# Optimization experiments

Measured on AMD Instinct MI355X. Metric: run time of the kernel, lower is better.

Reference implementation:

```python
import jax, jax.numpy as jnp
import numpy as np

B, N, D, H = 256, 100000, 512, 2048

def setup_inputs() -> dict:
    key = jax.random.key(0)
    ks = jax.random.split(key, 8)
    scale = 0.02
    return {
        "codes": jax.random.normal(ks[0], (B, D), jnp.float32),
        "codes_table": jax.random.normal(ks[1], (N, D), jnp.float32),
        "w1": jax.random.normal(ks[2], (D, H), jnp.float32) * scale,
        "b1": jnp.zeros((H,), jnp.float32),
        "w2u": jax.random.normal(ks[3], (H, D), jnp.float32) * scale,
        "b2u": jnp.zeros((D,), jnp.float32),
        "w2s": jax.random.normal(ks[4], (H, D), jnp.float32) * scale,
        "b2s": jnp.zeros((D,), jnp.float32),
        "k": 5,
    }

def reference(codes, codes_table, w1, b1, w2u, b2u, w2s, b2s, k):
    x_sq = jnp.sum(codes * codes, axis=1, keepdims=True)          # [B, 1]
    c_sq = jnp.sum(codes_table * codes_table, axis=1)             # [N]
    d2 = x_sq - 2.0 * (codes @ codes_table.T) + c_sq[None, :]     # [B, N]
    dists = jnp.sqrt(jnp.maximum(d2, 0.0))
    # smallest-k via top_k of negated distances
    neg_top, neighbor_idx = jax.lax.top_k(-dists, k)              # [B, k]
    # eval mode: chosen_neighbor_index = 0 (nearest neighbor)
    prev_code = codes_table[neighbor_idx[:, 0]]                   # [B, D]
    # encode MLP
    h1 = jax.nn.relu(prev_code @ w1 + b1)                         # [B, H]
    mu = h1 @ w2u + b2u                                           # [B, D]
    logstd = h1 @ w2s + b2s                                       # [B, D]
    return (mu, logstd)
```

## Files before the change

### kernel.cpp

```cpp
#include <hip/hip_runtime.h>
#include <hip/hip_bf16.h>
#include <cstdint>

typedef __attribute__((ext_vector_type(8))) short short8;
typedef __attribute__((ext_vector_type(16))) float f32x16;

constexpr int M   = 256;
constexpr int NTB = 100000;
constexpr int D   = 512;
constexpr int H   = 2048;

constexpr int BROWS = 128;
constexpr int NBLK  = (NTB + BROWS - 1) / BROWS;
constexpr float EPS_MARGIN = 4.0f;

constexpr size_t WS_CODES_HI = 0;
constexpr size_t WS_KEYS     = 262144;
constexpr size_t WS_IDX      = WS_KEYS + (size_t)M * NBLK * 8;
constexpr size_t WS_H1       = WS_IDX + 1024;

__device__ inline unsigned short f2bf_rne(float x) {
  unsigned u = __float_as_uint(x);
  u += 0x7fffu + ((u >> 16) & 1u);
  return (unsigned short)(u >> 16);
}
__device__ inline unsigned long long packkey(float s, unsigned n) {
  unsigned u = __float_as_uint(s);
  u = (u & 0x80000000u) ? ~u : (u | 0x80000000u);
  return ((unsigned long long)u << 32) | n;
}
__device__ inline float unpackf(unsigned u) {
  u = (u & 0x80000000u) ? (u & 0x7fffffffu) : ~u;
  return __uint_as_float(u);
}
__device__ inline unsigned long long u64min(unsigned long long a, unsigned long long b) {
  return a < b ? a : b;
}

__global__ __launch_bounds__(256) void convert_codes_kernel(
    const float* __restrict__ codes, unsigned short* __restrict__ chi)
{
  const int i = blockIdx.x * 256 + threadIdx.x;
  const int q = i >> 9, k = i & 511;
  const int g = q >> 5, s = k >> 4;
  const int lane = (q & 31) | (((k >> 3) & 1) << 5);
  const int j = k & 7;
  chi[((size_t)(g * 32 + s) * 64 + (size_t)lane) * 8 + j] = f2bf_rne(codes[i]);
}

__global__ __launch_bounds__(512) void dist_mfma_kernel(
    const float* __restrict__ table,
    const unsigned short* __restrict__ chi,
    unsigned long long* __restrict__ keys)
{
  __shared__ short8 AsH[2][4][2][64];
  __shared__ float csq_s[BROWS];
  __shared__ unsigned long long mrg[4][64];

  const int t    = threadIdx.x;
  const int lane = t & 63;
  const int w    = t >> 6;
  const int wr   = w >> 2;
  const int wc   = w & 3;
  const int blk  = blockIdx.x;

  const int srow = t >> 2;
  const int sk   = (t & 3) * 8;
  const int grow = min(blk * BROWS + srow, NTB - 1);
  const float* gsrc = table + (size_t)grow * D + sk;
  const int msub_w = srow >> 5;
  const int s_w    = sk >> 4;
  const int lpos   = (((sk >> 3) & 1) << 5) | (srow & 31);

  const unsigned short* bhp[2];
  #pragma unroll
  for (int nt = 0; nt < 2; ++nt)
    bhp[nt] = chi + (size_t)(wc * 2 + nt) * 16384 + (size_t)lane * 8;

  f32x16 acc[2][2];
  #pragma unroll
  for (int a = 0; a < 2; ++a)
    #pragma unroll
    for (int b = 0; b < 2; ++b)
      #pragma unroll
      for (int r = 0; r < 16; ++r) acc[a][b][r] = 0.f;

  float csq = 0.f;
  float4 p0, p1;

  p0 = *(const float4*)(gsrc);
  p1 = *(const float4*)(gsrc + 4);
  {
    float xs[8] = {p0.x,p0.y,p0.z,p0.w,p1.x,p1.y,p1.z,p1.w};
    short8 vh;
    #pragma unroll
    for (int j = 0; j < 8; ++j) {
      csq += xs[j] * xs[j];
      vh[j] = (short)f2bf_rne(xs[j]);
    }
    AsH[0][msub_w][s_w][lpos] = vh;
  }
  __syncthreads();

  for (int kt = 0; kt < 16; ++kt) {
    const int cur = kt & 1;
    if (kt < 15) {
      p0 = *(const float4*)(gsrc + (kt + 1) * 32);
      p1 = *(const float4*)(gsrc + (kt + 1) * 32 + 4);
    }
    #pragma unroll
    for (int s = 0; s < 2; ++s) {
      const int sg = kt * 2 + s;
      short8 aH[2], bH[2];
      #pragma unroll
      for (int mt = 0; mt < 2; ++mt) aH[mt] = AsH[cur][wr * 2 + mt][s][lane];
      #pragma unroll
      for (int nt = 0; nt < 2; ++nt) bH[nt] = *(const short8*)(bhp[nt] + (size_t)sg * 512);
      #pragma unroll
      for (int mt = 0; mt < 2; ++mt)
        #pragma unroll
        for (int nt = 0; nt < 2; ++nt)
          acc[mt][nt] = __builtin_amdgcn_mfma_f32_32x32x16_bf16(aH[mt], bH[nt], acc[mt][nt], 0, 0, 0);
    }
    if (kt < 15) {
      float xs[8] = {p0.x,p0.y,p0.z,p0.w,p1.x,p1.y,p1.z,p1.w};
      short8 vh;
      #pragma unroll
      for (int j = 0; j < 8; ++j) {
        csq += xs[j] * xs[j];
        vh[j] = (short)f2bf_rne(xs[j]);
      }
      AsH[cur ^ 1][msub_w][s_w][lpos] = vh;
    }
    __syncthreads();
  }

  csq += __shfl_xor(csq, 1);
  csq += __shfl_xor(csq, 2);
  if ((t & 3) == 0) csq_s[srow] = csq;
  __syncthreads();

  unsigned long long bestq[2];
  #pragma unroll
  for (int nt = 0; nt < 2; ++nt) {
    unsigned long long best = ~0ull;
    #pragma unroll
    for (int mt = 0; mt < 2; ++mt) {
      #pragma unroll
      for (int r = 0; r < 16; ++r) {
        const int lrow = wr * 64 + mt * 32 + (r & 3) + ((r >> 2) * 8) + ((lane >> 5) * 4);
        const int gr = blk * BROWS + lrow;
        if (gr < NTB) {
          const float sc = csq_s[lrow] - 2.f * acc[mt][nt][r];
          best = u64min(best, packkey(sc, (unsigned)gr));
        }
      }
    }
    best = u64min(best, __shfl_xor(best, 32));
    bestq[nt] = best;
  }
  if (wr == 1 && lane < 32) {
    mrg[wc][lane]      = bestq[0];
    mrg[wc][32 + lane] = bestq[1];
  }
  __syncthreads();
  if (wr == 0 && lane < 32) {
    #pragma unroll
    for (int nt = 0; nt < 2; ++nt) {
      const unsigned long long b = u64min(bestq[nt], mrg[wc][nt * 32 + lane]);
      const int q = wc * 64 + nt * 32 + lane;
      keys[(size_t)q * NBLK + blk] = b;
    }
  }
}

__global__ __launch_bounds__(256) void merge_rescore_kernel(
    const unsigned long long* __restrict__ keys,
    const float* __restrict__ codes, const float* __restrict__ table,
    unsigned* __restrict__ out_idx)
{
  __shared__ unsigned long long wmin[4];
  __shared__ unsigned long long bestkey_s;
  __shared__ int cand[16];
  __shared__ int ncand;
  __shared__ float redbuf[4];
  __shared__ float bestv_s;
  __shared__ int   besti_s;

  const int q = blockIdx.x, t = threadIdx.x;
  const unsigned long long* row = keys + (size_t)q * NBLK;

  unsigned long long lb = ~0ull;
  for (int i = t; i < NBLK; i += 256) lb = u64min(lb, row[i]);
  #pragma unroll
  for (int off = 1; off < 64; off <<= 1) lb = u64min(lb, __shfl_xor(lb, off));
  if ((t & 63) == 0) wmin[t >> 6] = lb;
  __syncthreads();
  if (t == 0) {
    unsigned long long b = u64min(u64min(wmin[0], wmin[1]), u64min(wmin[2], wmin[3]));
    bestkey_s = b;
    cand[0] = (int)(b & 0xffffffffu);
    ncand = 1;
  }
  __syncthreads();
  const unsigned long long bk = bestkey_s;
  const float thr = unpackf((unsigned)(bk >> 32)) + EPS_MARGIN;
  for (int i = t; i < NBLK; i += 256) {
    unsigned long long v = row[i];
    if (v != bk && unpackf((unsigned)(v >> 32)) <= thr) {
      int p = atomicAdd(&ncand, 1);
      if (p < 16) cand[p] = (int)(v & 0xffffffffu);
    }
  }
  __syncthreads();
  const int nc = min(ncand, 16);
  if (nc == 1) {
    if (t == 0) out_idx[q] = (unsigned)cand[0];
    return;
  }
  if (t == 0) { bestv_s = INFINITY; besti_s = 0x7fffffff; }
  __syncthreads();
  for (int c = 0; c < nc; ++c) {
    const int n = cand[c];
    const float* crow = table + (size_t)n * D;
    const float* xrow = codes + (size_t)q * D;
    float part = 0.f;
    for (int d = t; d < D; d += 256) part += crow[d] * crow[d] - 2.f * xrow[d] * crow[d];
    #pragma unroll
    for (int off = 1; off < 64; off <<= 1) part += __shfl_xor(part, off);
    if ((t & 63) == 0) redbuf[t >> 6] = part;
    __syncthreads();
    if (t == 0) {
      float tot = redbuf[0] + redbuf[1] + redbuf[2] + redbuf[3];
      if (tot < bestv_s || (tot == bestv_s && n < besti_s)) { bestv_s = tot; besti_s = n; }
    }
    __syncthreads();
  }
  if (t == 0) out_idx[q] = (unsigned)besti_s;
}

constexpr int BM2 = 64, BN2 = 64, BK2 = 16;

__global__ __launch_bounds__(256) void mlp1_kernel(
    const unsigned* __restrict__ final_idx,
    const float* __restrict__ table,
    const float* __restrict__ w1, const float* __restrict__ b1,
    float* __restrict__ h1)
{
  __shared__ float As[2][BK2][BM2];
  __shared__ float Bs[2][BK2][BN2];
  __shared__ unsigned idx_s[BM2];

  const int t  = threadIdx.x;
  const int tx = t & 15, ty = t >> 4;
  const int h0 = blockIdx.x * BN2;
  const int m0 = blockIdx.y * BM2;

  if (t < BM2) idx_s[t] = final_idx[m0 + t];
  __syncthreads();

  const int mr = t >> 2, c4 = (t & 3) * 4;
  const int dd = t >> 4, cb = (t & 15) * 4;
  const float* arow = table + (size_t)idx_s[mr] * D + c4;
  const float* brow = w1 + (size_t)dd * H + h0 + cb;

  float acc[4][4] = {{0.f}};

  float4 av = *(const float4*)(arow);
  float4 bv = *(const float4*)(brow);
  {
    float a[4] = {av.x, av.y, av.z, av.w};
    #pragma unroll
    for (int j = 0; j < 4; ++j) As[0][c4 + j][mr] = a[j];
    *(float4*)&Bs[0][dd][cb] = bv;
  }
  __syncthreads();

  for (int kt = 0; kt < D / BK2; ++kt) {
    const int cur = kt & 1;
    if (kt < D / BK2 - 1) {
      av = *(const float4*)(arow + (kt + 1) * BK2);
      bv = *(const float4*)(brow + (size_t)(kt + 1) * BK2 * H);
    }
    #pragma unroll
    for (int kk = 0; kk < BK2; ++kk) {
      float4 a4 = *(const float4*)&As[cur][kk][ty * 4];
      float4 b4 = *(const float4*)&Bs[cur][kk][tx * 4];
      float a[4] = {a4.x,a4.y,a4.z,a4.w}, b[4] = {b4.x,b4.y,b4.z,b4.w};
      #pragma unroll
      for (int i = 0; i < 4; ++i)
        #pragma unroll
        for (int j = 0; j < 4; ++j) acc[i][j] += a[i] * b[j];
    }
    if (kt < D / BK2 - 1) {
      float a[4] = {av.x, av.y, av.z, av.w};
      #pragma unroll
      for (int j = 0; j < 4; ++j) As[cur ^ 1][c4 + j][mr] = a[j];
      *(float4*)&Bs[cur ^ 1][dd][cb] = bv;
    }
    __syncthreads();
  }

  #pragma unroll
  for (int i = 0; i < 4; ++i) {
    const int m = m0 + ty * 4 + i;
    float v0 = acc[i][0] + b1[h0 + tx * 4 + 0];
    float v1 = acc[i][1] + b1[h0 + tx * 4 + 1];
    float v2 = acc[i][2] + b1[h0 + tx * 4 + 2];
    float v3 = acc[i][3] + b1[h0 + tx * 4 + 3];
    float4 o;
    o.x = v0 > 0.f ? v0 : 0.f;
    o.y = v1 > 0.f ? v1 : 0.f;
    o.z = v2 > 0.f ? v2 : 0.f;
    o.w = v3 > 0.f ? v3 : 0.f;
    *(float4*)(h1 + (size_t)m * H + h0 + tx * 4) = o;
  }
}

__global__ void init_out_kernel(const float* __restrict__ b2u,
                                const float* __restrict__ b2s,
                                float* __restrict__ out)
{
  const int i = blockIdx.x * blockDim.x + threadIdx.x;
  if (i < M * D) out[i] = b2u[i & (D - 1)];
  else           out[i] = b2s[i & (D - 1)];
}

constexpr int KSPLIT = 4;

__global__ __launch_bounds__(256) void mlp2_kernel(
    const float* __restrict__ h1,
    const float* __restrict__ w2u, const float* __restrict__ w2s,
    float* __restrict__ out)
{
  __shared__ float As[2][BK2][BM2];
  __shared__ float Bs[2][BK2][BN2];

  const int t  = threadIdx.x;
  const int tx = t & 15, ty = t >> 4;
  const int n0 = blockIdx.x * BN2;
  const int m0 = blockIdx.y * BM2;
  const int k0 = blockIdx.z * (H / KSPLIT);

  const float* Wn = (n0 < D) ? w2u : w2s;
  const int col0 = n0 & (D - 1);

  const int mr = t >> 2, c4 = (t & 3) * 4;
  const int dd = t >> 4, cb = (t & 15) * 4;
  const float* arow = h1 + (size_t)(m0 + mr) * H + k0 + c4;
  const float* brow = Wn + (size_t)(k0 + dd) * D + col0 + cb;

  float acc[4][4] = {{0.f}};
  constexpr int NITER = (H / KSPLIT) / BK2;

  float4 av = *(const float4*)(arow);
  float4 bv = *(const float4*)(brow);
  {
    float a[4] = {av.x, av.y, av.z, av.w};
    #pragma unroll
    for (int j = 0; j < 4; ++j) As[0][c4 + j][mr] = a[j];
    *(float4*)&Bs[0][dd][cb] = bv;
  }
  __syncthreads();

  for (int kt = 0; kt < NITER; ++kt) {
    const int cur = kt & 1;
    if (kt < NITER - 1) {
      av = *(const float4*)(arow + (kt + 1) * BK2);
      bv = *(const float4*)(brow + (size_t)(kt + 1) * BK2 * D);
    }
    #pragma unroll
    for (int kk = 0; kk < BK2; ++kk) {
      float4 a4 = *(const float4*)&As[cur][kk][ty * 4];
      float4 b4 = *(const float4*)&Bs[cur][kk][tx * 4];
      float a[4] = {a4.x,a4.y,a4.z,a4.w}, b[4] = {b4.x,b4.y,b4.z,b4.w};
      #pragma unroll
      for (int i = 0; i < 4; ++i)
        #pragma unroll
        for (int j = 0; j < 4; ++j) acc[i][j] += a[i] * b[j];
    }
    if (kt < NITER - 1) {
      float a[4] = {av.x, av.y, av.z, av.w};
      #pragma unroll
      for (int j = 0; j < 4; ++j) As[cur ^ 1][c4 + j][mr] = a[j];
      *(float4*)&Bs[cur ^ 1][dd][cb] = bv;
    }
    __syncthreads();
  }

  #pragma unroll
  for (int i = 0; i < 4; ++i) {
    const int m = m0 + ty * 4 + i;
    const int c = col0 + tx * 4;
    float* dst = (n0 < D) ? (out + (size_t)m * D + c)
                          : (out + (size_t)(M * D) + (size_t)m * D + c);
    #pragma unroll
    for (int j = 0; j < 4; ++j) atomicAdd(dst + j, acc[i][j]);
  }
}

extern "C" void kernel_launch(void* const* d_in, const int* in_sizes, int n_in,
                              void* d_out, int out_size, void* d_ws, size_t ws_size,
                              hipStream_t stream)
{
  const float* codes = (const float*)d_in[0];
  const float* table = (const float*)d_in[1];
  const float* w1    = (const float*)d_in[2];
  const float* b1    = (const float*)d_in[3];
  const float* w2u   = (const float*)d_in[4];
  const float* b2u   = (const float*)d_in[5];
  const float* w2s   = (const float*)d_in[6];
  const float* b2s   = (const float*)d_in[7];
  float* out = (float*)d_out;

  unsigned short* chi = (unsigned short*)((char*)d_ws + WS_CODES_HI);
  unsigned long long* keys = (unsigned long long*)((char*)d_ws + WS_KEYS);
  unsigned* final_idx = (unsigned*)((char*)d_ws + WS_IDX);
  float* h1 = (float*)((char*)d_ws + WS_H1);

  convert_codes_kernel<<<(M * D) / 256, 256, 0, stream>>>(codes, chi);

  dist_mfma_kernel<<<NBLK, 512, 0, stream>>>(table, chi, keys);

  merge_rescore_kernel<<<M, 256, 0, stream>>>(keys, codes, table, final_idx);

  dim3 gB1(H / BN2, M / BM2);
  mlp1_kernel<<<gB1, 256, 0, stream>>>(final_idx, table, w1, b1, h1);

  init_out_kernel<<<(2 * M * D) / 256, 256, 0, stream>>>(b2u, b2s, out);

  dim3 gB2((2 * D) / BN2, M / BM2, KSPLIT);
  mlp2_kernel<<<gB2, 256, 0, stream>>>(h1, w2u, w2s, out);
}
```

Before: 143.2 us.

## Deepen global-load prefetch to three stages and register-prefetch B fragments in distance GEMM

The distance kernel now loads table rows three k-tiles ahead into a triple-buffered LDS ring instead of one tile ahead with double buffering. It also prefetches the next B (codes) fragment from global memory into registers before issuing the current MFMAs, and fully unrolls the k-loop. The aim is to hide global memory latency on the streamed 100000x512 table and on the B reads behind matrix work. In exchange it uses more registers and LDS, which may reduce occupancy.

```diff
diff --git a/kernel.cpp b/kernel.cpp
--- a/kernel.cpp
+++ b/kernel.cpp
@@ -53,7 +53,7 @@
     const unsigned short* __restrict__ chi,
     unsigned long long* __restrict__ keys)
 {
-  __shared__ short8 AsH[2][4][2][64];
+  __shared__ short8 AsH[3][4][2][64];
   __shared__ float csq_s[BROWS];
   __shared__ unsigned long long mrg[4][64];
 
@@ -86,54 +86,58 @@
       for (int r = 0; r < 16; ++r) acc[a][b][r] = 0.f;
 
   float csq = 0.f;
-  float4 p0, p1;
-
-  p0 = *(const float4*)(gsrc);
-  p1 = *(const float4*)(gsrc + 4);
-  {
-    float xs[8] = {p0.x,p0.y,p0.z,p0.w,p1.x,p1.y,p1.z,p1.w};
-    short8 vh;
-    #pragma unroll
-    for (int j = 0; j < 8; ++j) {
-      csq += xs[j] * xs[j];
-      vh[j] = (short)f2bf_rne(xs[j]);
-    }
-    AsH[0][msub_w][s_w][lpos] = vh;
-  }
-  __syncthreads();
-
+  float4 pa[3], pb[3];
+
+#define CONV(T) do {                                                      \
+    float xs[8] = {pa[(T) % 3].x, pa[(T) % 3].y, pa[(T) % 3].z, pa[(T) % 3].w, \
+                   pb[(T) % 3].x, pb[(T) % 3].y, pb[(T) % 3].z, pb[(T) % 3].w}; \
+    short8 vh;                                                            \
+    _Pragma("unroll")                                                     \
+    for (int j = 0; j < 8; ++j) {                                         \
+      csq += xs[j] * xs[j];                                               \
+      vh[j] = (short)f2bf_rne(xs[j]);                                     \
+    }                                                                     \
+    AsH[(T) % 3][msub_w][s_w][lpos] = vh;                                 \
+  } while (0)
+
+  #pragma unroll
+  for (int pre = 0; pre < 3; ++pre) {
+    pa[pre] = *(const float4*)(gsrc + pre * 32);
+    pb[pre] = *(const float4*)(gsrc + pre * 32 + 4);
+  }
+  CONV(0);
+  __syncthreads();
+
+  short8 bcur[2];
+  bcur[0] = *(const short8*)(bhp[0]);
+  bcur[1] = *(const short8*)(bhp[1]);
+
+  #pragma unroll
   for (int kt = 0; kt < 16; ++kt) {
-    const int cur = kt & 1;
-    if (kt < 15) {
-      p0 = *(const float4*)(gsrc + (kt + 1) * 32);
-      p1 = *(const float4*)(gsrc + (kt + 1) * 32 + 4);
+    if (kt + 3 < 16) {
+      pa[kt % 3] = *(const float4*)(gsrc + (kt + 3) * 32);
+      pb[kt % 3] = *(const float4*)(gsrc + (kt + 3) * 32 + 4);
     }
     #pragma unroll
     for (int s = 0; s < 2; ++s) {
       const int sg = kt * 2 + s;
-      short8 aH[2], bH[2];
-      #pragma unroll
-      for (int mt = 0; mt < 2; ++mt) aH[mt] = AsH[cur][wr * 2 + mt][s][lane];
-      #pragma unroll
-      for (int nt = 0; nt < 2; ++nt) bH[nt] = *(const short8*)(bhp[nt] + (size_t)sg * 512);
-      #pragma unroll
-      for (int mt = 0; mt < 2; ++mt)
-        #pragma unroll
-        for (int nt = 0; nt < 2; ++nt)
-          acc[mt][nt] = __builtin_amdgcn_mfma_f32_32x32x16_bf16(aH[mt], bH[nt], acc[mt][nt], 0, 0, 0);
-    }
-    if (kt < 15) {
-      float xs[8] = {p0.x,p0.y,p0.z,p0.w,p1.x,p1.y,p1.z,p1.w};
-      short8 vh;
-      #pragma unroll
-      for (int j = 0; j < 8; ++j) {
-        csq += xs[j] * xs[j];
-        vh[j] = (short)f2bf_rne(xs[j]);
+      short8 aH[2], bnx[2];
+      aH[0] = AsH[kt % 3][wr * 2 + 0][s][lane];
+      aH[1] = AsH[kt % 3][wr * 2 + 1][s][lane];
+      if (sg < 31) {
+        bnx[0] = *(const short8*)(bhp[0] + (size_t)(sg + 1) * 512);
+        bnx[1] = *(const short8*)(bhp[1] + (size_t)(sg + 1) * 512);
       }
-      AsH[cur ^ 1][msub_w][s_w][lpos] = vh;
-    }
+      acc[0][0] = __builtin_amdgcn_mfma_f32_32x32x16_bf16(aH[0], bcur[0], acc[0][0], 0, 0, 0);
+      acc[0][1] = __builtin_amdgcn_mfma_f32_32x32x16_bf16(aH[0], bcur[1], acc[0][1], 0, 0, 0);
+      acc[1][0] = __builtin_amdgcn_mfma_f32_32x32x16_bf16(aH[1], bcur[0], acc[1][0], 0, 0, 0);
+      acc[1][1] = __builtin_amdgcn_mfma_f32_32x32x16_bf16(aH[1], bcur[1], acc[1][1], 0, 0, 0);
+      if (sg < 31) { bcur[0] = bnx[0]; bcur[1] = bnx[1]; }
+    }
+    if (kt + 1 < 16) CONV(kt + 1);
     __syncthreads();
   }
+#undef CONV
 
   csq += __shfl_xor(csq, 1);
   csq += __shfl_xor(csq, 2);
```

After: 147.9 us. 1.03x slower.

## Restructure distance kernel to per-wave 32-row strips with register-only pipelining

Applied to the files above, without the earlier changes.

Each wave now owns a 32-row strip of the table and computes its distances against all 256 queries using 8 accumulator tiles. Table rows are read straight from global memory into registers through a 4-deep prefetch, which removes the LDS staging buffer and the per-k-step block barriers. Query fragments are also prefetched one step ahead. The keys layout becomes strip-major, so the merge kernel now does strided reads. This raises register pressure (8 f32x16 accumulators) and reloads the query matrix once per wave instead of once per block.

```diff
diff --git a/kernel.cpp b/kernel.cpp
--- a/kernel.cpp
+++ b/kernel.cpp
@@ -10,13 +10,14 @@
 constexpr int D   = 512;
 constexpr int H   = 2048;
 
-constexpr int BROWS = 128;
-constexpr int NBLK  = (NTB + BROWS - 1) / BROWS;
+constexpr int NSTRIP = NTB / 32;
+constexpr int WPB    = 4;
+constexpr int NBLK_D = (NSTRIP + WPB - 1) / WPB;
 constexpr float EPS_MARGIN = 4.0f;
 
 constexpr size_t WS_CODES_HI = 0;
 constexpr size_t WS_KEYS     = 262144;
-constexpr size_t WS_IDX      = WS_KEYS + (size_t)M * NBLK * 8;
+constexpr size_t WS_IDX      = WS_KEYS + (size_t)NSTRIP * 256 * 8;
 constexpr size_t WS_H1       = WS_IDX + 1024;
 
 __device__ inline unsigned short f2bf_rne(float x) {
@@ -48,129 +49,92 @@
   chi[((size_t)(g * 32 + s) * 64 + (size_t)lane) * 8 + j] = f2bf_rne(codes[i]);
 }
 
-__global__ __launch_bounds__(512) void dist_mfma_kernel(
+__global__ __launch_bounds__(256, 2) void dist_mfma_kernel(
     const float* __restrict__ table,
     const unsigned short* __restrict__ chi,
     unsigned long long* __restrict__ keys)
 {
-  __shared__ short8 AsH[2][4][2][64];
-  __shared__ float csq_s[BROWS];
-  __shared__ unsigned long long mrg[4][64];
+  __shared__ float csqw[WPB][32];
 
   const int t    = threadIdx.x;
   const int lane = t & 63;
   const int w    = t >> 6;
-  const int wr   = w >> 2;
-  const int wc   = w & 3;
-  const int blk  = blockIdx.x;
-
-  const int srow = t >> 2;
-  const int sk   = (t & 3) * 8;
-  const int grow = min(blk * BROWS + srow, NTB - 1);
-  const float* gsrc = table + (size_t)grow * D + sk;
-  const int msub_w = srow >> 5;
-  const int s_w    = sk >> 4;
-  const int lpos   = (((sk >> 3) & 1) << 5) | (srow & 31);
-
-  const unsigned short* bhp[2];
-  #pragma unroll
-  for (int nt = 0; nt < 2; ++nt)
-    bhp[nt] = chi + (size_t)(wc * 2 + nt) * 16384 + (size_t)lane * 8;
-
-  f32x16 acc[2][2];
-  #pragma unroll
-  for (int a = 0; a < 2; ++a)
-    #pragma unroll
-    for (int b = 0; b < 2; ++b)
-      #pragma unroll
-      for (int r = 0; r < 16; ++r) acc[a][b][r] = 0.f;
+  const int half = lane >> 5;
+  const int r32  = lane & 31;
+
+  int strip = blockIdx.x * WPB + w;
+  if (strip >= NSTRIP) strip = NSTRIP - 1;
+  const int row_base = strip * 32;
+
+  const float* asrc = table + (size_t)(row_base + r32) * D + half * 8;
+  const int voff = lane * 8;
+
+  f32x16 acc[8];
+  #pragma unroll
+  for (int nt = 0; nt < 8; ++nt)
+    #pragma unroll
+    for (int r = 0; r < 16; ++r) acc[nt][r] = 0.f;
+
+  float4 aq[4][2];
+  short8 bq[8];
+
+  #pragma unroll
+  for (int i = 0; i < 4; ++i) {
+    aq[i][0] = *(const float4*)(asrc + i * 16);
+    aq[i][1] = *(const float4*)(asrc + i * 16 + 4);
+  }
+  #pragma unroll
+  for (int nt = 0; nt < 8; ++nt)
+    bq[nt] = *(const short8*)(chi + (size_t)nt * 16384 + voff);
 
   float csq = 0.f;
-  float4 p0, p1;
-
-  p0 = *(const float4*)(gsrc);
-  p1 = *(const float4*)(gsrc + 4);
-  {
-    float xs[8] = {p0.x,p0.y,p0.z,p0.w,p1.x,p1.y,p1.z,p1.w};
-    short8 vh;
-    #pragma unroll
-    for (int j = 0; j < 8; ++j) {
-      csq += xs[j] * xs[j];
-      vh[j] = (short)f2bf_rne(xs[j]);
-    }
-    AsH[0][msub_w][s_w][lpos] = vh;
-  }
-  __syncthreads();
-
-  for (int kt = 0; kt < 16; ++kt) {
-    const int cur = kt & 1;
-    if (kt < 15) {
-      p0 = *(const float4*)(gsrc + (kt + 1) * 32);
-      p1 = *(const float4*)(gsrc + (kt + 1) * 32 + 4);
-    }
-    #pragma unroll
-    for (int s = 0; s < 2; ++s) {
-      const int sg = kt * 2 + s;
-      short8 aH[2], bH[2];
-      #pragma unroll
-      for (int mt = 0; mt < 2; ++mt) aH[mt] = AsH[cur][wr * 2 + mt][s][lane];
-      #pragma unroll
-      for (int nt = 0; nt < 2; ++nt) bH[nt] = *(const short8*)(bhp[nt] + (size_t)sg * 512);
-      #pragma unroll
-      for (int mt = 0; mt < 2; ++mt)
-        #pragma unroll
-        for (int nt = 0; nt < 2; ++nt)
-          acc[mt][nt] = __builtin_amdgcn_mfma_f32_32x32x16_bf16(aH[mt], bH[nt], acc[mt][nt], 0, 0, 0);
-    }
-    if (kt < 15) {
-      float xs[8] = {p0.x,p0.y,p0.z,p0.w,p1.x,p1.y,p1.z,p1.w};
-      short8 vh;
+
+  #pragma unroll 4
+  for (int kt = 0; kt < 32; ++kt) {
+    const int slot = kt & 3;
+    short8 aH;
+    {
+      float xs[8] = {aq[slot][0].x, aq[slot][0].y, aq[slot][0].z, aq[slot][0].w,
+                     aq[slot][1].x, aq[slot][1].y, aq[slot][1].z, aq[slot][1].w};
       #pragma unroll
       for (int j = 0; j < 8; ++j) {
         csq += xs[j] * xs[j];
-        vh[j] = (short)f2bf_rne(xs[j]);
+        aH[j] = (short)f2bf_rne(xs[j]);
       }
-      AsH[cur ^ 1][msub_w][s_w][lpos] = vh;
-    }
-    __syncthreads();
-  }
-
-  csq += __shfl_xor(csq, 1);
-  csq += __shfl_xor(csq, 2);
-  if ((t & 3) == 0) csq_s[srow] = csq;
-  __syncthreads();
-
-  unsigned long long bestq[2];
-  #pragma unroll
-  for (int nt = 0; nt < 2; ++nt) {
+    }
+    if (kt + 4 < 32) {
+      aq[slot][0] = *(const float4*)(asrc + (kt + 4) * 16);
+      aq[slot][1] = *(const float4*)(asrc + (kt + 4) * 16 + 4);
+    }
+    #pragma unroll
+    for (int nt = 0; nt < 8; ++nt) {
+      acc[nt] = __builtin_amdgcn_mfma_f32_32x32x16_bf16(aH, bq[nt], acc[nt], 0, 0, 0);
+      if (kt + 1 < 32)
+        bq[nt] = *(const short8*)(chi + (size_t)nt * 16384 + (kt + 1) * 512 + voff);
+    }
+  }
+
+  csq += __shfl_xor(csq, 32);
+  if (half == 0) csqw[w][r32] = csq;
+  __syncthreads();
+
+  float csq_r[16];
+  #pragma unroll
+  for (int r = 0; r < 16; ++r)
+    csq_r[r] = csqw[w][(r & 3) + 8 * (r >> 2) + 4 * half];
+
+  #pragma unroll
+  for (int nt = 0; nt < 8; ++nt) {
     unsigned long long best = ~0ull;
     #pragma unroll
-    for (int mt = 0; mt < 2; ++mt) {
-      #pragma unroll
-      for (int r = 0; r < 16; ++r) {
-        const int lrow = wr * 64 + mt * 32 + (r & 3) + ((r >> 2) * 8) + ((lane >> 5) * 4);
-        const int gr = blk * BROWS + lrow;
-        if (gr < NTB) {
-          const float sc = csq_s[lrow] - 2.f * acc[mt][nt][r];
-          best = u64min(best, packkey(sc, (unsigned)gr));
-        }
-      }
+    for (int r = 0; r < 16; ++r) {
+      const int grow = row_base + (r & 3) + 8 * (r >> 2) + 4 * half;
+      const float sc = csq_r[r] - 2.f * acc[nt][r];
+      best = u64min(best, packkey(sc, (unsigned)grow));
     }
     best = u64min(best, __shfl_xor(best, 32));
-    bestq[nt] = best;
-  }
-  if (wr == 1 && lane < 32) {
-    mrg[wc][lane]      = bestq[0];
-    mrg[wc][32 + lane] = bestq[1];
-  }
-  __syncthreads();
-  if (wr == 0 && lane < 32) {
-    #pragma unroll
-    for (int nt = 0; nt < 2; ++nt) {
-      const unsigned long long b = u64min(bestq[nt], mrg[wc][nt * 32 + lane]);
-      const int q = wc * 64 + nt * 32 + lane;
-      keys[(size_t)q * NBLK + blk] = b;
-    }
+    if (half == 0)
+      keys[(size_t)strip * 256 + nt * 32 + r32] = best;
   }
 }
 
@@ -188,10 +152,9 @@
   __shared__ int   besti_s;
 
   const int q = blockIdx.x, t = threadIdx.x;
-  const unsigned long long* row = keys + (size_t)q * NBLK;
 
   unsigned long long lb = ~0ull;
-  for (int i = t; i < NBLK; i += 256) lb = u64min(lb, row[i]);
+  for (int i = t; i < NSTRIP; i += 256) lb = u64min(lb, keys[(size_t)i * 256 + q]);
   #pragma unroll
   for (int off = 1; off < 64; off <<= 1) lb = u64min(lb, __shfl_xor(lb, off));
   if ((t & 63) == 0) wmin[t >> 6] = lb;
@@ -205,8 +168,8 @@
   __syncthreads();
   const unsigned long long bk = bestkey_s;
   const float thr = unpackf((unsigned)(bk >> 32)) + EPS_MARGIN;
-  for (int i = t; i < NBLK; i += 256) {
-    unsigned long long v = row[i];
+  for (int i = t; i < NSTRIP; i += 256) {
+    unsigned long long v = keys[(size_t)i * 256 + q];
     if (v != bk && unpackf((unsigned)(v >> 32)) <= thr) {
       int p = atomicAdd(&ncand, 1);
       if (p < 16) cand[p] = (int)(v & 0xffffffffu);
@@ -420,7 +383,7 @@
 
   convert_codes_kernel<<<(M * D) / 256, 256, 0, stream>>>(codes, chi);
 
-  dist_mfma_kernel<<<NBLK, 512, 0, stream>>>(table, chi, keys);
+  dist_mfma_kernel<<<NBLK_D, 256, 0, stream>>>(table, chi, keys);
 
   merge_rescore_kernel<<<M, 256, 0, stream>>>(keys, codes, table, final_idx);
 
```

Measured after the change: 275.4 us. +92.2%, slower.
